# Optimization experiments

Hardware: AMD Instinct MI355X
Metric: run time of the kernel (lower is better)

The kernel has to match this reference:

```python
import jax, jax.numpy as jnp
import numpy as np

B, S, D, E, H, K = 2, 2048, 1024, 8, 4096, 2


def setup_inputs() -> dict:
    key = jax.random.key(0)
    ks = jax.random.split(key, 7)
    sd = 1.0 / np.sqrt(D)
    sh = 1.0 / np.sqrt(H)
    return {
        "x": jax.random.normal(ks[0], (B, S, D), dtype=jnp.float32),
        "router_w": jax.random.uniform(ks[1], (D, E), jnp.float32, -sd, sd),
        "router_b": jnp.zeros((E,), jnp.float32),
        "w1": jax.random.uniform(ks[2], (E, D, H), jnp.float32, -sd, sd),
        "b1": jnp.zeros((E, H), jnp.float32),
        "w2": jax.random.uniform(ks[3], (E, H, D), jnp.float32, -sh, sh),
        "b2": jnp.zeros((E, D), jnp.float32),
    }


def reference(x, router_w, router_b, w1, b1, w2, b2):
    # Router: softmax over experts, then top-k and renormalize
    router_logits = jnp.einsum("bsd,de->bse", x, router_w) + router_b
    router_probs = jax.nn.softmax(router_logits, axis=-1)
    top_k_probs, top_k_indices = jax.lax.top_k(router_probs, K)  # [B,S,K]
    top_k_probs = top_k_probs / jnp.sum(top_k_probs, axis=-1, keepdims=True)

    # Dense all-expert FFN (Block assumed: Linear -> GELU -> Linear)
    h = jax.nn.gelu(jnp.einsum("bsd,edh->bseh", x, w1) + b1)  # [B,S,E,H]
    expert_outputs = jnp.einsum("bseh,ehd->bsed", h, w2) + b2  # [B,S,E,D]

    # Gather top-k experts per token and combine with renormalized probs
    idx = top_k_indices[..., None]  # [B,S,K,1]
    selected = jnp.take_along_axis(expert_outputs, idx, axis=2)  # [B,S,K,D]
    return jnp.sum(selected * top_k_probs[..., None], axis=2)  # [B,S,D]
```

## Files before the change

### kernel.cpp

```cpp
#include <hip/hip_runtime.h>
#include <hip/hip_bf16.h>

#define TOK   4096
#define DDIM  1024
#define NEXP  8
#define HDIM  4096
#define KSEL  2
#define NPAIR (TOK * KSEL)
#define NSPLIT 4

typedef __attribute__((ext_vector_type(8))) _Float16 f16x8;
typedef __attribute__((ext_vector_type(4))) _Float16 f16x4;
typedef __attribute__((ext_vector_type(4))) float    f32x4;

__device__ __forceinline__ void gload16(const void* g, void* l) {
  __builtin_amdgcn_global_load_lds((const __attribute__((address_space(1))) void*)g,
                                   (__attribute__((address_space(3))) void*)l, 16, 0, 0);
}

__device__ __forceinline__ float gelu_tanh(float u) {
  float inner = 0.7978845608028654f * (u + 0.044715f * u * u * u);
  float t2 = __expf(2.f * inner);
  return u - u / (t2 + 1.f);
}

__global__ __launch_bounds__(256) void k_router(const float* __restrict__ x,
    const float* __restrict__ rw, const float* __restrict__ rb,
    int* __restrict__ tidx, float* __restrict__ tw,
    _Float16* __restrict__ xb) {
  const int t    = blockIdx.x * 4 + (threadIdx.x >> 6);
  const int lane = threadIdx.x & 63;
  const float* xr = x + (size_t)t * DDIM;
  _Float16*   xbr = xb + (size_t)t * DDIM;
  float acc[NEXP];
#pragma unroll
  for (int e = 0; e < NEXP; ++e) acc[e] = 0.f;
  for (int d0 = lane * 4; d0 < DDIM; d0 += 256) {
    const float4 xv = *(const float4*)(xr + d0);
    f16x4 hx;
    hx[0] = (_Float16)xv.x; hx[1] = (_Float16)xv.y;
    hx[2] = (_Float16)xv.z; hx[3] = (_Float16)xv.w;
    *(f16x4*)(xbr + d0) = hx;
#pragma unroll
    for (int i = 0; i < 4; ++i) {
      const float xs = (&xv.x)[i];
      const float4 r0 = *(const float4*)(rw + (size_t)(d0 + i) * NEXP);
      const float4 r1 = *(const float4*)(rw + (size_t)(d0 + i) * NEXP + 4);
      acc[0] += xs * r0.x; acc[1] += xs * r0.y; acc[2] += xs * r0.z; acc[3] += xs * r0.w;
      acc[4] += xs * r1.x; acc[5] += xs * r1.y; acc[6] += xs * r1.z; acc[7] += xs * r1.w;
    }
  }
#pragma unroll
  for (int e = 0; e < NEXP; ++e) {
    float v = acc[e];
#pragma unroll
    for (int s = 32; s; s >>= 1) v += __shfl_xor(v, s, 64);
    acc[e] = v;
  }
  if (lane == 0) {
    float lg[NEXP];
#pragma unroll
    for (int e = 0; e < NEXP; ++e) lg[e] = acc[e] + rb[e];
    int i0 = 0;
#pragma unroll
    for (int e = 1; e < NEXP; ++e) if (lg[e] > lg[i0]) i0 = e;
    int i1 = -1; float best = -3.4e38f;
#pragma unroll
    for (int e = 0; e < NEXP; ++e) {
      if (e == i0) continue;
      if (lg[e] > best) { best = lg[e]; i1 = e; }
    }
    float w0 = 1.f / (1.f + expf(lg[i1] - lg[i0]));
    tidx[t * 2]     = i0;  tidx[t * 2 + 1] = i1;
    tw[t * 2]       = w0;  tw[t * 2 + 1]   = 1.f - w0;
  }
}

__global__ __launch_bounds__(1024) void k_scan(const int* __restrict__ tidx,
                       const float* __restrict__ tw,
                       int* __restrict__ offs,
                       int* __restrict__ row_token, float* __restrict__ row_w,
                       int* __restrict__ inv) {
  __shared__ int hist[NEXP];
  __shared__ int soff[NEXP + 1];
  __shared__ int scur[NEXP];
  if (threadIdx.x < NEXP) hist[threadIdx.x] = 0;
  __syncthreads();
  const int lane = threadIdx.x & 63;
  int e_loc[NPAIR / 1024];
#pragma unroll
  for (int it = 0; it < NPAIR / 1024; ++it) {
    const int p = it * 1024 + threadIdx.x;
    const int e = tidx[p];
    e_loc[it] = e;
#pragma unroll
    for (int ee = 0; ee < NEXP; ++ee) {
      unsigned long long m = __ballot(e == ee);
      if (m && lane == 0) atomicAdd(&hist[ee], __popcll(m));
    }
  }
  __syncthreads();
  if (threadIdx.x == 0) {
    int run = 0;
    for (int e = 0; e < NEXP; ++e) { soff[e] = run; scur[e] = run; run += hist[e]; }
    soff[NEXP] = run;
    for (int e = 0; e <= NEXP; ++e) offs[e] = soff[e];
  }
  __syncthreads();
#pragma unroll
  for (int it = 0; it < NPAIR / 1024; ++it) {
    const int p = it * 1024 + threadIdx.x;
    const int e = e_loc[it];
    int pos = 0;
#pragma unroll
    for (int ee = 0; ee < NEXP; ++ee) {
      unsigned long long m = __ballot(e == ee);
      if (!m) continue;
      int base = 0;
      if (lane == 0) base = atomicAdd(&scur[ee], __popcll(m));
      base = __shfl(base, 0, 64);
      if (e == ee) pos = base + __popcll(m & ((1ull << lane) - 1ull));
    }
    row_token[pos] = p >> 1;
    row_w[pos]     = tw[p];
    inv[p]         = pos;
  }
}

__global__ __launch_bounds__(256) void k_transpose2(const float* __restrict__ w1,
    const float* __restrict__ w2, _Float16* __restrict__ w1t, _Float16* __restrict__ w2t) {
  __shared__ _Float16 tile[64][72];
  const int zz = blockIdx.y;
  const float* ip; _Float16* op; int Rr, Cc, i0, j0;
  if (zz < NEXP) {
    ip = w1 + (size_t)zz * DDIM * HDIM;  op = w1t + (size_t)zz * DDIM * HDIM;
    Rr = DDIM; Cc = HDIM;
    i0 = (blockIdx.x >> 6) * 64; j0 = (blockIdx.x & 63) * 64;
  } else {
    ip = w2 + (size_t)(zz - NEXP) * HDIM * DDIM;  op = w2t + (size_t)(zz - NEXP) * HDIM * DDIM;
    Rr = HDIM; Cc = DDIM;
    i0 = (blockIdx.x >> 4) * 64; j0 = (blockIdx.x & 15) * 64;
  }
  const int tx = threadIdx.x & 15, ty = threadIdx.x >> 4;
#pragma unroll
  for (int rr = 0; rr < 4; ++rr) {
    int r = ty + rr * 16;
    float4 v = *(const float4*)(ip + (size_t)(i0 + r) * Cc + j0 + tx * 4);
    tile[r][tx * 4 + 0] = (_Float16)v.x;
    tile[r][tx * 4 + 1] = (_Float16)v.y;
    tile[r][tx * 4 + 2] = (_Float16)v.z;
    tile[r][tx * 4 + 3] = (_Float16)v.w;
  }
  __syncthreads();
#pragma unroll
  for (int cc = 0; cc < 4; ++cc) {
    int c = ty + cc * 16;
    f16x4 o;
#pragma unroll
    for (int k = 0; k < 4; ++k) o[k] = tile[tx * 4 + k][c];
    *(f16x4*)(op + (size_t)(j0 + c) * Rr + i0 + tx * 4) = o;
  }
}

#define BM 128
#define BN 128
#define BK 64


__global__ __launch_bounds__(256) void k_gemm1(
    const _Float16* __restrict__ xb,
    const _Float16* __restrict__ w1t,
    const float* __restrict__ b1,
    const int* __restrict__ offs,
    const int* __restrict__ row_token,
    _Float16* __restrict__ hbuf) {
  const int e    = blockIdx.z;
  const int off0 = offs[e];
  const int ne   = offs[e + 1] - off0;
  const int m0   = blockIdx.y * BM;
  if (m0 >= ne) return;
  const int n0   = blockIdx.x * BN;
  const int mrem = ne - m0;

  __shared__ __align__(16) char smem[32768];
  char* As = smem;
  char* Bs = smem + 16384;

  const int tid = threadIdx.x;
  const int wv = tid >> 6, lane = tid & 63;
  const int l15 = lane & 15;
  const int wr = wv >> 1, wc = wv & 1;
  const int lr = lane >> 3;
  const unsigned ssl = (unsigned)(((lane & 7) ^ lr) << 4);

  const char* a_c = (const char*)xb;
  const char* b_c = (const char*)(w1t + (size_t)e * HDIM * DDIM);

  size_t apB[4], bpB[4];
#pragma unroll
  for (int i = 0; i < 4; ++i) {
    int r  = wv * 32 + i * 8 + lr;
    int rc = (r < mrem) ? r : (mrem - 1);
    apB[i] = (size_t)row_token[off0 + m0 + rc] * (DDIM * 2) + ssl;
    bpB[i] = (size_t)(n0 + r) * (DDIM * 2) + ssl;
  }

  f32x4 acc[4][4] = {};
  const int NT = DDIM / BK;

  for (int ks = 0; ks < NT; ++ks) {
    const size_t kb = (size_t)ks * 128;
#pragma unroll
    for (int i = 0; i < 4; ++i) {
      gload16(a_c + apB[i] + kb, As + (wv * 32 + i * 8) * 128);
      gload16(b_c + bpB[i] + kb, Bs + (wv * 32 + i * 8) * 128);
    }
    __syncthreads();
#pragma unroll
    for (int kk = 0; kk < 2; ++kk) {
      f16x8 af[4], bfr[4];
      const unsigned rsl = (unsigned)((kk * 4 + (lane >> 4)) ^ (l15 & 7)) << 4;
#pragma unroll
      for (int m = 0; m < 4; ++m)
        af[m] = *(const f16x8*)(As + (wr * 64 + m * 16 + l15) * 128 + rsl);
#pragma unroll
      for (int n = 0; n < 4; ++n)
        bfr[n] = *(const f16x8*)(Bs + (wc * 64 + n * 16 + l15) * 128 + rsl);
#pragma unroll
      for (int m = 0; m < 4; ++m)
#pragma unroll
        for (int n = 0; n < 4; ++n)
          acc[m][n] = __builtin_amdgcn_mfma_f32_16x16x32_f16(af[m], bfr[n], acc[m][n], 0, 0, 0);
    }
    __syncthreads();
  }

  float bias[4];
#pragma unroll
  for (int n = 0; n < 4; ++n)
    bias[n] = b1[(size_t)e * HDIM + n0 + wc * 64 + n * 16 + l15];
#pragma unroll
  for (int m = 0; m < 4; ++m) {
#pragma unroll
    for (int j = 0; j < 4; ++j) {
      int row = wr * 64 + m * 16 + (lane >> 4) * 4 + j;
#pragma unroll
      for (int n = 0; n < 4; ++n) {
        int col = wc * 64 + n * 16 + l15;
        *(_Float16*)(smem + (row << 8) + (((col << 1) ^ ((row & 15) << 4)))) =
            (_Float16)gelu_tanh(acc[m][n][j] + bias[n]);
      }
    }
  }
  __syncthreads();
  {
    const int srow = tid >> 1, half = tid & 1;
    if (srow < mrem) {
      _Float16* hr = hbuf + (size_t)(off0 + m0 + srow) * HDIM + n0 + half * 64;
#pragma unroll
      for (int i = 0; i < 8; ++i) {
        f16x8 v = *(const f16x8*)(smem + (srow << 8) + (((half * 128 + i * 16) ^ ((srow & 15) << 4))));
        *(f16x8*)(hr + i * 8) = v;
      }
    }
  }
}

template <bool YB>
__global__ __launch_bounds__(256) void k_gemm2(
    const _Float16* __restrict__ hbuf,
    const _Float16* __restrict__ w2t,
    const float* __restrict__ b2,
    const int* __restrict__ offs,
    const int* __restrict__ row_token,
    const float* __restrict__ row_w,
    _Float16* __restrict__ yb,
    float* __restrict__ out) {
  const int zz = blockIdx.z;
  const int e  = zz >> 2;
  const int kh = zz & 3;
  const int off0 = offs[e];
  const int ne   = offs[e + 1] - off0;
  const int m0   = blockIdx.y * BM;
  if (m0 >= ne) return;
  const int n0   = blockIdx.x * BN;
  const int mrem = ne - m0;

  __shared__ __align__(16) char smem[32768];
  char* As = smem;
  char* Bs = smem + 16384;

  const int tid = threadIdx.x;
  const int wv = tid >> 6, lane = tid & 63;
  const int l15 = lane & 15;
  const int wr = wv >> 1, wc = wv & 1;
  const int lr = lane >> 3;
  const unsigned ssl = (unsigned)(((lane & 7) ^ lr) << 4);

  const char* a_c = (const char*)hbuf;
  const char* b_c = (const char*)(w2t + (size_t)e * DDIM * HDIM);
  const size_t khb = (size_t)kh * ((HDIM / NSPLIT) * 2);

  size_t apB[4], bpB[4];
#pragma unroll
  for (int i = 0; i < 4; ++i) {
    int r  = wv * 32 + i * 8 + lr;
    int rc = (r < mrem) ? r : (mrem - 1);
    apB[i] = (size_t)(off0 + m0 + rc) * (HDIM * 2) + khb + ssl;
    bpB[i] = (size_t)(n0 + r) * (HDIM * 2) + khb + ssl;
  }

  f32x4 acc[4][4] = {};
  const int NT = (HDIM / NSPLIT) / BK;

  for (int ks = 0; ks < NT; ++ks) {
    const size_t kb = (size_t)ks * 128;
#pragma unroll
    for (int i = 0; i < 4; ++i) {
      gload16(a_c + apB[i] + kb, As + (wv * 32 + i * 8) * 128);
      gload16(b_c + bpB[i] + kb, Bs + (wv * 32 + i * 8) * 128);
    }
    __syncthreads();
#pragma unroll
    for (int kk = 0; kk < 2; ++kk) {
      f16x8 af[4], bfr[4];
      const unsigned rsl = (unsigned)((kk * 4 + (lane >> 4)) ^ (l15 & 7)) << 4;
#pragma unroll
      for (int m = 0; m < 4; ++m)
        af[m] = *(const f16x8*)(As + (wr * 64 + m * 16 + l15) * 128 + rsl);
#pragma unroll
      for (int n = 0; n < 4; ++n)
        bfr[n] = *(const f16x8*)(Bs + (wc * 64 + n * 16 + l15) * 128 + rsl);
#pragma unroll
      for (int m = 0; m < 4; ++m)
#pragma unroll
        for (int n = 0; n < 4; ++n)
          acc[m][n] = __builtin_amdgcn_mfma_f32_16x16x32_f16(af[m], bfr[n], acc[m][n], 0, 0, 0);
    }
    __syncthreads();
  }

  if (YB) {
    _Float16* ypart = yb + (size_t)kh * NPAIR * DDIM;
#pragma unroll
    for (int m = 0; m < 4; ++m) {
#pragma unroll
      for (int j = 0; j < 4; ++j) {
        int row = wr * 64 + m * 16 + (lane >> 4) * 4 + j;
#pragma unroll
        for (int n = 0; n < 4; ++n) {
          int col = wc * 64 + n * 16 + l15;
          *(_Float16*)(smem + (row << 8) + (((col << 1) ^ ((row & 15) << 4)))) =
              (_Float16)acc[m][n][j];
        }
      }
    }
    __syncthreads();
    const int srow = tid >> 1, half = tid & 1;
    if (srow < mrem) {
      _Float16* yr = ypart + (size_t)(off0 + m0 + srow) * DDIM + n0 + half * 64;
#pragma unroll
      for (int i = 0; i < 8; ++i) {
        f16x8 v = *(const f16x8*)(smem + (srow << 8) + (((half * 128 + i * 16) ^ ((srow & 15) << 4))));
        *(f16x8*)(yr + i * 8) = v;
      }
    }
  } else {
    float bias[4];
#pragma unroll
    for (int n = 0; n < 4; ++n)
      bias[n] = (kh == 0) ? b2[(size_t)e * DDIM + n0 + wc * 64 + n * 16 + l15] : 0.f;
#pragma unroll
    for (int m = 0; m < 4; ++m) {
#pragma unroll
      for (int j = 0; j < 4; ++j) {
        int row = wr * 64 + m * 16 + (lane >> 4) * 4 + j;
        if (row < mrem) {
          int g = off0 + m0 + row;
          float wgt = row_w[g];
          float* op = out + (size_t)row_token[g] * DDIM + n0 + wc * 64 + l15;
#pragma unroll
          for (int n = 0; n < 4; ++n)
            atomicAdd(op + n * 16, wgt * (acc[m][n][j] + bias[n]));
        }
      }
    }
  }
}

__global__ __launch_bounds__(256) void k_combine(const _Float16* __restrict__ yb,
    const int* __restrict__ inv, const int* __restrict__ tidx,
    const float* __restrict__ tw, const float* __restrict__ b2,
    float* __restrict__ out) {
  const int t  = blockIdx.x * 2 + (threadIdx.x >> 7);
  const int c8 = (threadIdx.x & 127) * 8;
  const int g0 = inv[2 * t],  g1 = inv[2 * t + 1];
  const int e0 = tidx[2 * t], e1 = tidx[2 * t + 1];
  const float w0 = tw[2 * t], w1 = tw[2 * t + 1];
  float s0[8] = {0,0,0,0,0,0,0,0}, s1[8] = {0,0,0,0,0,0,0,0};
#pragma unroll
  for (int p = 0; p < NSPLIT; ++p) {
    const _Float16* yp = yb + (size_t)p * NPAIR * DDIM;
    f16x8 a = *(const f16x8*)(yp + (size_t)g0 * DDIM + c8);
    f16x8 b = *(const f16x8*)(yp + (size_t)g1 * DDIM + c8);
#pragma unroll
    for (int i = 0; i < 8; ++i) { s0[i] += (float)a[i]; s1[i] += (float)b[i]; }
  }
  float o[8];
#pragma unroll
  for (int i = 0; i < 8; ++i) {
    float bA = b2[(size_t)e0 * DDIM + c8 + i];
    float bB = b2[(size_t)e1 * DDIM + c8 + i];
    o[i] = w0 * (s0[i] + bA) + w1 * (s1[i] + bB);
  }
  float* op = out + (size_t)t * DDIM + c8;
  *(float4*)op       = make_float4(o[0], o[1], o[2], o[3]);
  *(float4*)(op + 4) = make_float4(o[4], o[5], o[6], o[7]);
}

extern "C" void kernel_launch(void* const* d_in, const int* in_sizes, int n_in,
                              void* d_out, int out_size, void* d_ws, size_t ws_size,
                              hipStream_t stream) {
  const float* x  = (const float*)d_in[0];
  const float* rw = (const float*)d_in[1];
  const float* rb = (const float*)d_in[2];
  const float* w1 = (const float*)d_in[3];
  const float* b1 = (const float*)d_in[4];
  const float* w2 = (const float*)d_in[5];
  const float* b2 = (const float*)d_in[6];
  float* out = (float*)d_out;
  char* ws = (char*)d_ws;

  int*      tidx    = (int*)(ws + 0);
  float*    tw      = (float*)(ws + 32768);
  int*      offs    = (int*)(ws + 65792);
  int*      row_tok = (int*)(ws + 66048);
  float*    row_w   = (float*)(ws + 98816);
  int*      inv     = (int*)(ws + 131584);
  _Float16* xb      = (_Float16*)(ws + 164352);
  _Float16* wtA     = (_Float16*)(ws + 8552960);
  _Float16* wtB     = (_Float16*)(ws + 75661824);
  _Float16* hb      = (_Float16*)(ws + 142770688);
  _Float16* yb      = wtA;
  const bool big = ws_size >= 209879552ULL;

  if (!big) hipMemsetAsync(out, 0, (size_t)TOK * DDIM * sizeof(float), stream);

  k_router<<<dim3(TOK / 4), 256, 0, stream>>>(x, rw, rb, tidx, tw, xb);
  k_scan<<<dim3(1), 1024, 0, stream>>>(tidx, tw, offs, row_tok, row_w, inv);
  k_transpose2<<<dim3(1024, 2 * NEXP), 256, 0, stream>>>(w1, w2, wtA, wtB);
  k_gemm1<<<dim3(HDIM / BN, TOK / BM, NEXP), 256, 0, stream>>>(xb, wtA, b1, offs, row_tok, hb);
  if (big) {
    k_gemm2<true><<<dim3(DDIM / BN, TOK / BM, NEXP * NSPLIT), 256, 0, stream>>>(
        hb, wtB, b2, offs, row_tok, row_w, yb, out);
    k_combine<<<dim3(TOK / 2), 256, 0, stream>>>(yb, inv, tidx, tw, b2, out);
  } else {
    k_gemm2<false><<<dim3(DDIM / BN, TOK / BM, NEXP * NSPLIT), 256, 0, stream>>>(
        hb, wtB, b2, offs, row_tok, row_w, yb, out);
  }
}
```

Measured before the change: 400.5 us.

## Replace both expert GEMMs with a 256x256 pipelined LDS double-buffered kernel

Merges the two grouped expert GEMMs into one templated kernel that uses 256x256 output tiles, 512 threads and 128 KB of LDS. It prefetches the next K-tiles through global_load_lds while issuing MFMAs, controlled by explicit vmcnt waits, barriers and s_setprio. The aim is to raise data reuse per tile and hide global-load latency behind the matrix math. The atomic-add fallback for small workspaces is dropped, so the yb partial buffer plus the combine kernel is now always used. In exchange, LDS use and register pressure go up, which likely limits occupancy to one block per CU.

```diff
diff --git a/kernel.cpp b/kernel.cpp
--- a/kernel.cpp
+++ b/kernel.cpp
@@ -162,227 +162,166 @@
   }
 }
 
-#define BM 128
-#define BN 128
-#define BK 64
-
-
-__global__ __launch_bounds__(256) void k_gemm1(
-    const _Float16* __restrict__ xb,
-    const _Float16* __restrict__ w1t,
-    const float* __restrict__ b1,
+template <bool G1>
+__global__ __launch_bounds__(512, 2) void k_gemm256(
+    const _Float16* __restrict__ A,
+    const _Float16* __restrict__ Bw,
+    const float* __restrict__ bias_g,
     const int* __restrict__ offs,
     const int* __restrict__ row_token,
-    _Float16* __restrict__ hbuf) {
-  const int e    = blockIdx.z;
+    _Float16* __restrict__ outb) {
+  const int e    = G1 ? blockIdx.z : (blockIdx.z >> 2);
+  const int kh   = G1 ? 0 : (blockIdx.z & 3);
   const int off0 = offs[e];
   const int ne   = offs[e + 1] - off0;
-  const int m0   = blockIdx.y * BM;
+  const int m0   = blockIdx.y * 256;
   if (m0 >= ne) return;
-  const int n0   = blockIdx.x * BN;
+  const int n0   = blockIdx.x * 256;
   const int mrem = ne - m0;
 
-  __shared__ __align__(16) char smem[32768];
-  char* As = smem;
-  char* Bs = smem + 16384;
+  constexpr int RSTR = G1 ? (DDIM * 2) : (HDIM * 2);
+  constexpr int OSTR = G1 ? HDIM : DDIM;
+
+  __shared__ __align__(16) char smem[131072];
 
   const int tid = threadIdx.x;
-  const int wv = tid >> 6, lane = tid & 63;
-  const int l15 = lane & 15;
-  const int wr = wv >> 1, wc = wv & 1;
-  const int lr = lane >> 3;
-  const unsigned ssl = (unsigned)(((lane & 7) ^ lr) << 4);
-
-  const char* a_c = (const char*)xb;
-  const char* b_c = (const char*)(w1t + (size_t)e * HDIM * DDIM);
-
-  size_t apB[4], bpB[4];
-#pragma unroll
-  for (int i = 0; i < 4; ++i) {
-    int r  = wv * 32 + i * 8 + lr;
-    int rc = (r < mrem) ? r : (mrem - 1);
-    apB[i] = (size_t)row_token[off0 + m0 + rc] * (DDIM * 2) + ssl;
-    bpB[i] = (size_t)(n0 + r) * (DDIM * 2) + ssl;
-  }
-
-  f32x4 acc[4][4] = {};
-  const int NT = DDIM / BK;
-
-  for (int ks = 0; ks < NT; ++ks) {
-    const size_t kb = (size_t)ks * 128;
-#pragma unroll
-    for (int i = 0; i < 4; ++i) {
-      gload16(a_c + apB[i] + kb, As + (wv * 32 + i * 8) * 128);
-      gload16(b_c + bpB[i] + kb, Bs + (wv * 32 + i * 8) * 128);
-    }
-    __syncthreads();
-#pragma unroll
-    for (int kk = 0; kk < 2; ++kk) {
-      f16x8 af[4], bfr[4];
-      const unsigned rsl = (unsigned)((kk * 4 + (lane >> 4)) ^ (l15 & 7)) << 4;
-#pragma unroll
-      for (int m = 0; m < 4; ++m)
-        af[m] = *(const f16x8*)(As + (wr * 64 + m * 16 + l15) * 128 + rsl);
-#pragma unroll
-      for (int n = 0; n < 4; ++n)
-        bfr[n] = *(const f16x8*)(Bs + (wc * 64 + n * 16 + l15) * 128 + rsl);
-#pragma unroll
-      for (int m = 0; m < 4; ++m)
-#pragma unroll
-        for (int n = 0; n < 4; ++n)
-          acc[m][n] = __builtin_amdgcn_mfma_f32_16x16x32_f16(af[m], bfr[n], acc[m][n], 0, 0, 0);
-    }
-    __syncthreads();
-  }
-
-  float bias[4];
-#pragma unroll
-  for (int n = 0; n < 4; ++n)
-    bias[n] = b1[(size_t)e * HDIM + n0 + wc * 64 + n * 16 + l15];
-#pragma unroll
-  for (int m = 0; m < 4; ++m) {
+  const int wid = tid >> 6, lane = tid & 63;
+  const int wm = wid >> 2, wn = wid & 3;
+  const int l15 = lane & 15, l16 = lane >> 4;
+  const unsigned khb = (unsigned)kh * 2048u;
+
+  const int r0 = tid >> 3, sl = tid & 7;
+  const int r1 = 64 + r0;
+  const unsigned d0 = (unsigned)tid * 16u;
+  const unsigned d1 = 8192u + (unsigned)tid * 16u;
+
+  unsigned arow[2][2], brow[2][2];
+#pragma unroll
+  for (int h = 0; h < 2; ++h) {
+    const int ga = 128 * h + r0, gb = 128 * h + r1;
+    const int ca = (ga < mrem) ? ga : (mrem - 1);
+    const int cb = (gb < mrem) ? gb : (mrem - 1);
+    if (G1) {
+      arow[h][0] = (unsigned)row_token[off0 + m0 + ca] * (unsigned)RSTR + (unsigned)((sl ^ (r0 & 7)) << 4);
+      arow[h][1] = (unsigned)row_token[off0 + m0 + cb] * (unsigned)RSTR + (unsigned)((sl ^ (r1 & 7)) << 4);
+    } else {
+      arow[h][0] = (unsigned)(off0 + m0 + ca) * (unsigned)RSTR + khb + (unsigned)((sl ^ (r0 & 7)) << 4);
+      arow[h][1] = (unsigned)(off0 + m0 + cb) * (unsigned)RSTR + khb + (unsigned)((sl ^ (r1 & 7)) << 4);
+    }
+    brow[h][0] = (unsigned)(n0 + 128 * h + r0) * (unsigned)RSTR + khb + (unsigned)((sl ^ (r0 & 7)) << 4);
+    brow[h][1] = (unsigned)(n0 + 128 * h + r1) * (unsigned)RSTR + khb + (unsigned)((sl ^ (r1 & 7)) << 4);
+  }
+
+  const char* a_c = (const char*)A;
+  const char* b_c = (const char*)(Bw + (size_t)e * (size_t)(HDIM * DDIM));
+
+#define ST_A(dst, h, kt) { gload16(a_c + arow[h][0] + (kt) * 128, smem + (dst) + d0); \
+                           gload16(a_c + arow[h][1] + (kt) * 128, smem + (dst) + d1); }
+#define ST_B(dst, h, kt) { gload16(b_c + brow[h][0] + (kt) * 128, smem + (dst) + d0); \
+                           gload16(b_c + brow[h][1] + (kt) * 128, smem + (dst) + d1); }
+
+  const unsigned aoff0 = (unsigned)(l15 * 128) + (unsigned)((((0 * 4) + l16) ^ (l15 & 7)) << 4);
+  const unsigned aoff1 = (unsigned)(l15 * 128) + (unsigned)((((1 * 4) + l16) ^ (l15 & 7)) << 4);
+
+  f32x4 acc[8][4] = {};
+
+  ST_A(0, 0, 0)       ST_A(16384, 1, 0)
+  ST_B(32768, 0, 0)   ST_B(49152, 1, 0)
+  ST_B(98304, 0, 1)   ST_B(114688, 1, 1)
+  asm volatile("s_waitcnt vmcnt(0)" ::: "memory");
+  __builtin_amdgcn_s_barrier();
+
+  for (int it = 0; it < 8; ++it) {
+    const bool more = (it < 7);
+    const int ktA1 = 2 * it + 1, ktN = 2 * it + 2, ktB1 = 2 * it + 3;
+#pragma unroll
+    for (int H = 0; H < 2; ++H) {
+      const char* Ar = smem + H * 65536 + wm * 16384;
+      const char* Br = smem + H * 65536 + 32768 + (wn >> 1) * 16384 + (wn & 1) * 8192;
+      f16x8 bfr[4][2];
+#pragma unroll
+      for (int q = 0; q < 4; ++q) {
+        if (q == 0) {
+#pragma unroll
+          for (int n = 0; n < 4; ++n) {
+            bfr[n][0] = *(const f16x8*)(Br + n * 2048 + aoff0);
+            bfr[n][1] = *(const f16x8*)(Br + n * 2048 + aoff1);
+          }
+        }
+        f16x8 af[2][2];
+#pragma unroll
+        for (int dm = 0; dm < 2; ++dm) {
+          af[dm][0] = *(const f16x8*)(Ar + (2 * q + dm) * 2048 + aoff0);
+          af[dm][1] = *(const f16x8*)(Ar + (2 * q + dm) * 2048 + aoff1);
+        }
+        if (H == 0) {
+          if (q == 0)      { ST_A(65536, 0, ktA1) }
+          else if (q == 1) { ST_A(81920, 1, ktA1) }
+          else if (q == 2) { if (more) ST_B(32768, 0, ktN) }
+          else             { if (more) ST_B(49152, 1, ktN) }
+        } else if (more) {
+          if (q == 0)      { ST_A(0, 0, ktN) }
+          else if (q == 1) { ST_A(16384, 1, ktN) }
+          else if (q == 2) { ST_B(98304, 0, ktB1) }
+          else             { ST_B(114688, 1, ktB1) }
+        }
+        __builtin_amdgcn_s_barrier();
+        __builtin_amdgcn_s_setprio(1);
+#pragma unroll
+        for (int dm = 0; dm < 2; ++dm)
+#pragma unroll
+          for (int n = 0; n < 4; ++n) {
+            acc[2 * q + dm][n] = __builtin_amdgcn_mfma_f32_16x16x32_f16(af[dm][0], bfr[n][0], acc[2 * q + dm][n], 0, 0, 0);
+            acc[2 * q + dm][n] = __builtin_amdgcn_mfma_f32_16x16x32_f16(af[dm][1], bfr[n][1], acc[2 * q + dm][n], 0, 0, 0);
+          }
+        __builtin_amdgcn_s_setprio(0);
+        if (q == 3) {
+          if (H == 0) {
+            if (more) { asm volatile("s_waitcnt vmcnt(4)" ::: "memory"); }
+            else      { asm volatile("s_waitcnt vmcnt(0)" ::: "memory"); }
+            __builtin_amdgcn_sched_barrier(0);
+          } else if (more) {
+            asm volatile("s_waitcnt vmcnt(4)" ::: "memory");
+            __builtin_amdgcn_sched_barrier(0);
+          }
+        }
+        __builtin_amdgcn_s_barrier();
+      }
+    }
+  }
+#undef ST_A
+#undef ST_B
+
+  float bv[4] = {0.f, 0.f, 0.f, 0.f};
+  if (G1) {
+#pragma unroll
+    for (int n = 0; n < 4; ++n)
+      bv[n] = bias_g[(size_t)e * HDIM + n0 + wn * 64 + n * 16 + l15];
+  }
+#pragma unroll
+  for (int m = 0; m < 8; ++m) {
 #pragma unroll
     for (int j = 0; j < 4; ++j) {
-      int row = wr * 64 + m * 16 + (lane >> 4) * 4 + j;
+      const int row = wm * 128 + m * 16 + l16 * 4 + j;
 #pragma unroll
       for (int n = 0; n < 4; ++n) {
-        int col = wc * 64 + n * 16 + l15;
-        *(_Float16*)(smem + (row << 8) + (((col << 1) ^ ((row & 15) << 4)))) =
-            (_Float16)gelu_tanh(acc[m][n][j] + bias[n]);
+        const int col = wn * 64 + n * 16 + l15;
+        float v = acc[m][n][j];
+        if (G1) v = gelu_tanh(v + bv[n]);
+        *(_Float16*)(smem + row * 512 + ((col * 2) ^ ((row & 15) << 4))) = (_Float16)v;
       }
     }
   }
   __syncthreads();
   {
-    const int srow = tid >> 1, half = tid & 1;
-    if (srow < mrem) {
-      _Float16* hr = hbuf + (size_t)(off0 + m0 + srow) * HDIM + n0 + half * 64;
-#pragma unroll
-      for (int i = 0; i < 8; ++i) {
-        f16x8 v = *(const f16x8*)(smem + (srow << 8) + (((half * 128 + i * 16) ^ ((srow & 15) << 4))));
-        *(f16x8*)(hr + i * 8) = v;
-      }
-    }
-  }
-}
-
-template <bool YB>
-__global__ __launch_bounds__(256) void k_gemm2(
-    const _Float16* __restrict__ hbuf,
-    const _Float16* __restrict__ w2t,
-    const float* __restrict__ b2,
-    const int* __restrict__ offs,
-    const int* __restrict__ row_token,
-    const float* __restrict__ row_w,
-    _Float16* __restrict__ yb,
-    float* __restrict__ out) {
-  const int zz = blockIdx.z;
-  const int e  = zz >> 2;
-  const int kh = zz & 3;
-  const int off0 = offs[e];
-  const int ne   = offs[e + 1] - off0;
-  const int m0   = blockIdx.y * BM;
-  if (m0 >= ne) return;
-  const int n0   = blockIdx.x * BN;
-  const int mrem = ne - m0;
-
-  __shared__ __align__(16) char smem[32768];
-  char* As = smem;
-  char* Bs = smem + 16384;
-
-  const int tid = threadIdx.x;
-  const int wv = tid >> 6, lane = tid & 63;
-  const int l15 = lane & 15;
-  const int wr = wv >> 1, wc = wv & 1;
-  const int lr = lane >> 3;
-  const unsigned ssl = (unsigned)(((lane & 7) ^ lr) << 4);
-
-  const char* a_c = (const char*)hbuf;
-  const char* b_c = (const char*)(w2t + (size_t)e * DDIM * HDIM);
-  const size_t khb = (size_t)kh * ((HDIM / NSPLIT) * 2);
-
-  size_t apB[4], bpB[4];
-#pragma unroll
-  for (int i = 0; i < 4; ++i) {
-    int r  = wv * 32 + i * 8 + lr;
-    int rc = (r < mrem) ? r : (mrem - 1);
-    apB[i] = (size_t)(off0 + m0 + rc) * (HDIM * 2) + khb + ssl;
-    bpB[i] = (size_t)(n0 + r) * (HDIM * 2) + khb + ssl;
-  }
-
-  f32x4 acc[4][4] = {};
-  const int NT = (HDIM / NSPLIT) / BK;
-
-  for (int ks = 0; ks < NT; ++ks) {
-    const size_t kb = (size_t)ks * 128;
-#pragma unroll
-    for (int i = 0; i < 4; ++i) {
-      gload16(a_c + apB[i] + kb, As + (wv * 32 + i * 8) * 128);
-      gload16(b_c + bpB[i] + kb, Bs + (wv * 32 + i * 8) * 128);
-    }
-    __syncthreads();
-#pragma unroll
-    for (int kk = 0; kk < 2; ++kk) {
-      f16x8 af[4], bfr[4];
-      const unsigned rsl = (unsigned)((kk * 4 + (lane >> 4)) ^ (l15 & 7)) << 4;
-#pragma unroll
-      for (int m = 0; m < 4; ++m)
-        af[m] = *(const f16x8*)(As + (wr * 64 + m * 16 + l15) * 128 + rsl);
-#pragma unroll
-      for (int n = 0; n < 4; ++n)
-        bfr[n] = *(const f16x8*)(Bs + (wc * 64 + n * 16 + l15) * 128 + rsl);
-#pragma unroll
-      for (int m = 0; m < 4; ++m)
-#pragma unroll
-        for (int n = 0; n < 4; ++n)
-          acc[m][n] = __builtin_amdgcn_mfma_f32_16x16x32_f16(af[m], bfr[n], acc[m][n], 0, 0, 0);
-    }
-    __syncthreads();
-  }
-
-  if (YB) {
-    _Float16* ypart = yb + (size_t)kh * NPAIR * DDIM;
-#pragma unroll
-    for (int m = 0; m < 4; ++m) {
-#pragma unroll
-      for (int j = 0; j < 4; ++j) {
-        int row = wr * 64 + m * 16 + (lane >> 4) * 4 + j;
-#pragma unroll
-        for (int n = 0; n < 4; ++n) {
-          int col = wc * 64 + n * 16 + l15;
-          *(_Float16*)(smem + (row << 8) + (((col << 1) ^ ((row & 15) << 4)))) =
-              (_Float16)acc[m][n][j];
-        }
-      }
-    }
-    __syncthreads();
-    const int srow = tid >> 1, half = tid & 1;
-    if (srow < mrem) {
-      _Float16* yr = ypart + (size_t)(off0 + m0 + srow) * DDIM + n0 + half * 64;
-#pragma unroll
-      for (int i = 0; i < 8; ++i) {
-        f16x8 v = *(const f16x8*)(smem + (srow << 8) + (((half * 128 + i * 16) ^ ((srow & 15) << 4))));
-        *(f16x8*)(yr + i * 8) = v;
-      }
-    }
-  } else {
-    float bias[4];
-#pragma unroll
-    for (int n = 0; n < 4; ++n)
-      bias[n] = (kh == 0) ? b2[(size_t)e * DDIM + n0 + wc * 64 + n * 16 + l15] : 0.f;
-#pragma unroll
-    for (int m = 0; m < 4; ++m) {
-#pragma unroll
-      for (int j = 0; j < 4; ++j) {
-        int row = wr * 64 + m * 16 + (lane >> 4) * 4 + j;
-        if (row < mrem) {
-          int g = off0 + m0 + row;
-          float wgt = row_w[g];
-          float* op = out + (size_t)row_token[g] * DDIM + n0 + wc * 64 + l15;
-#pragma unroll
-          for (int n = 0; n < 4; ++n)
-            atomicAdd(op + n * 16, wgt * (acc[m][n][j] + bias[n]));
-        }
+    const int row = tid >> 1, half = tid & 1;
+    if (row < mrem) {
+      _Float16* outp = (G1 ? outb : (outb + (size_t)kh * NPAIR * DDIM))
+                       + (size_t)(off0 + m0 + row) * OSTR + n0 + half * 128;
+#pragma unroll
+      for (int i = 0; i < 16; ++i) {
+        f16x8 v = *(const f16x8*)(smem + row * 512 + ((half * 256 + i * 16) ^ ((row & 15) << 4)));
+        *(f16x8*)(outp + i * 8) = v;
       }
     }
   }
@@ -442,20 +381,13 @@
   _Float16* wtB     = (_Float16*)(ws + 75661824);
   _Float16* hb      = (_Float16*)(ws + 142770688);
   _Float16* yb      = wtA;
-  const bool big = ws_size >= 209879552ULL;
-
-  if (!big) hipMemsetAsync(out, 0, (size_t)TOK * DDIM * sizeof(float), stream);
 
   k_router<<<dim3(TOK / 4), 256, 0, stream>>>(x, rw, rb, tidx, tw, xb);
   k_scan<<<dim3(1), 1024, 0, stream>>>(tidx, tw, offs, row_tok, row_w, inv);
   k_transpose2<<<dim3(1024, 2 * NEXP), 256, 0, stream>>>(w1, w2, wtA, wtB);
-  k_gemm1<<<dim3(HDIM / BN, TOK / BM, NEXP), 256, 0, stream>>>(xb, wtA, b1, offs, row_tok, hb);
-  if (big) {
-    k_gemm2<true><<<dim3(DDIM / BN, TOK / BM, NEXP * NSPLIT), 256, 0, stream>>>(
-        hb, wtB, b2, offs, row_tok, row_w, yb, out);
-    k_combine<<<dim3(TOK / 2), 256, 0, stream>>>(yb, inv, tidx, tw, b2, out);
-  } else {
-    k_gemm2<false><<<dim3(DDIM / BN, TOK / BM, NEXP * NSPLIT), 256, 0, stream>>>(
-        hb, wtB, b2, offs, row_tok, row_w, yb, out);
-  }
-}
+  k_gemm256<true><<<dim3(HDIM / 256, TOK / 256, NEXP), 512, 0, stream>>>(
+      xb, wtA, b1, offs, row_tok, hb);
+  k_gemm256<false><<<dim3(DDIM / 256, TOK / 256, NEXP * NSPLIT), 512, 0, stream>>>(
+      hb, wtB, b2, offs, row_tok, yb);
+  k_combine<<<dim3(TOK / 2), 256, 0, stream>>>(yb, inv, tidx, tw, b2, out);
+}
```

After: 391.0 us. 1.02x faster.
